# Kernel optimization log

Hardware: AMD Instinct MI355X
Metric: run time of the kernel (lower is better)

The kernel has to match this reference:

```python
import jax, jax.numpy as jnp
import numpy as np

D_IN = 1024
D_OUT = 1024
N_HEADS = 16
HEAD_DIM = D_IN // N_HEADS      # 64
HEAD_DIM_V = D_OUT // N_HEADS   # 64


def setup_inputs() -> dict:
    key = jax.random.key(0)
    ks = jax.random.split(key, 7)
    s = 0.02
    x = jax.random.normal(ks[0], (4, 2048, D_IN), dtype=jnp.float32)
    Wq = jax.random.normal(ks[1], (D_IN, D_IN), dtype=jnp.float32) * s
    bq = jnp.zeros((D_IN,), dtype=jnp.float32)
    Wk = jax.random.normal(ks[2], (D_IN, D_IN), dtype=jnp.float32) * s
    bk = jnp.zeros((D_IN,), dtype=jnp.float32)
    Wv = jax.random.normal(ks[3], (D_IN, D_OUT), dtype=jnp.float32) * s
    bv = jnp.zeros((D_OUT,), dtype=jnp.float32)
    return {"x": x, "Wq": Wq, "bq": bq, "Wk": Wk, "bk": bk, "Wv": Wv, "bv": bv}


def reference(x, Wq, bq, Wk, bk, Wv, bv):
    B, S, _ = x.shape
    scale = jnp.sqrt(jnp.asarray(HEAD_DIM, dtype=jnp.float32))
    # projections -> [B, S, H, Dh] -> [B, H, S, Dh]
    q = (x @ Wq + bq).reshape(B, S, N_HEADS, HEAD_DIM).transpose(0, 2, 1, 3)
    k = (x @ Wk + bk).reshape(B, S, N_HEADS, HEAD_DIM).transpose(0, 2, 1, 3)
    v = (x @ Wv + bv).reshape(B, S, N_HEADS, HEAD_DIM_V).transpose(0, 2, 1, 3)
    # [B, H, S, S] attention scores (naive full materialization, as in source)
    scores = jnp.einsum("bhsd,bhtd->bhst", q, k) / scale
    weights = jax.nn.softmax(scores, axis=-1)
    out = jnp.einsum("bhst,bhtd->bhsd", weights, v)
    # [B, H, S, Dv] -> [B, S, H*Dv]  (out_projection NOT applied in source forward)
    return out.transpose(0, 2, 1, 3).reshape(B, S, N_HEADS * HEAD_DIM_V)
```

## Files before the change

kernel.cpp:

```cpp
#include <hip/hip_runtime.h>

#define B_  4
#define S_  2048
#define D_  1024
#define H_  16
#define DH_ 64
#define M_  (B_ * S_)

typedef __attribute__((ext_vector_type(8))) short short8;
typedef __attribute__((ext_vector_type(4))) float floatx4;

__device__ __forceinline__ float bf2f(unsigned short u) {
    union { unsigned int i; float f; } v; v.i = ((unsigned int)u) << 16; return v.f;
}
__device__ __forceinline__ unsigned short f2bf(float f) {
    union { float f; unsigned int i; } v; v.f = f;
    unsigned int r = v.i + 0x7fffu + ((v.i >> 16) & 1u);
    return (unsigned short)(r >> 16);
}

typedef const __attribute__((address_space(1))) unsigned int* gas_ptr;
typedef __attribute__((address_space(3))) unsigned int* las_ptr;
__device__ __forceinline__ void async_cp16(const void* g, void* l) {
    __builtin_amdgcn_global_load_lds((gas_ptr)g, (las_ptr)l, 16, 0, 0);
}

__global__ __launch_bounds__(256) void cast_x_kernel(
    const float* __restrict__ x, unsigned short* __restrict__ Ax)
{
    int i4 = blockIdx.x * 256 + threadIdx.x;
    float4 v = reinterpret_cast<const float4*>(x)[i4];
    ushort4 o;
    o.x = f2bf(v.x); o.y = f2bf(v.y); o.z = f2bf(v.z); o.w = f2bf(v.w);
    reinterpret_cast<ushort4*>(Ax)[i4] = o;
}

__global__ __launch_bounds__(256) void cast_w_T_kernel(
    const float* __restrict__ W, unsigned short* __restrict__ Wt)
{
    __shared__ unsigned short T[64][72];
    const int t = threadIdx.x;
    const int k0 = blockIdx.x * 64, n0 = blockIdx.y * 64;

    #pragma unroll
    for (int p = 0; p < 4; ++p) {
        int kr = p * 16 + (t >> 4);
        int nc = (t & 15) * 4;
        float4 v = *reinterpret_cast<const float4*>(W + (size_t)(k0 + kr) * D_ + n0 + nc);
        T[nc + 0][kr] = f2bf(v.x);
        T[nc + 1][kr] = f2bf(v.y);
        T[nc + 2][kr] = f2bf(v.z);
        T[nc + 3][kr] = f2bf(v.w);
    }
    __syncthreads();

    const int nl = t >> 2, kc = (t & 3) * 16;
    size_t base = (size_t)(n0 + nl) * D_ + k0 + kc;
    *reinterpret_cast<short8*>(Wt + base)     = *reinterpret_cast<const short8*>(&T[nl][kc]);
    *reinterpret_cast<short8*>(Wt + base + 8) = *reinterpret_cast<const short8*>(&T[nl][kc + 8]);
}

__global__ __launch_bounds__(256) void gemm_qkv_mfma(
    const unsigned short* __restrict__ Ax,
    const unsigned short* __restrict__ Wtq,
    const unsigned short* __restrict__ Wtk,
    const unsigned short* __restrict__ Wtv,
    const float* __restrict__ bq, const float* __restrict__ bk,
    const float* __restrict__ bv,
    unsigned short* __restrict__ Q, unsigned short* __restrict__ K,
    unsigned short* __restrict__ Vtg)
{
    __shared__ unsigned short As[128 * 32];
    __shared__ unsigned short Bs[128 * 32];

    const int tid = threadIdx.x;
    const int lane = tid & 63;
    const int w = tid >> 6;
    const int wm = (w >> 1) * 64, wn = (w & 1) * 64;
    const int l15 = lane & 15, quad = lane >> 4;

    const int hw   = blockIdx.x;
    const int xcd  = hw & 7;
    const int slot = hw >> 3;
    const int gcol = xcd * 3 + slot % 3;
    const int m0   = (slot / 3) * 128;
    const int n0   = (gcol & 7) * 128;
    const int mat  = gcol >> 3;

    const unsigned short* Wt = mat == 0 ? Wtq : (mat == 1 ? Wtk : Wtv);
    const float* bias        = mat == 0 ? bq  : (mat == 1 ? bk  : bv);

    const int arow = tid >> 2;
    const int acol = (tid & 3) * 8;

    floatx4 acc[4][4] = {};

    for (int kb = 0; kb < 32; ++kb) {
        int cb = kb * 32;
        __syncthreads();
        async_cp16(Ax + (size_t)(m0 + arow) * D_ + cb + acol,      As + arow * 32 + acol);
        async_cp16(Ax + (size_t)(m0 + 64 + arow) * D_ + cb + acol, As + (64 + arow) * 32 + acol);
        async_cp16(Wt + (size_t)(n0 + arow) * D_ + cb + acol,      Bs + arow * 32 + acol);
        async_cp16(Wt + (size_t)(n0 + 64 + arow) * D_ + cb + acol, Bs + (64 + arow) * 32 + acol);
        __syncthreads();

        short8 af[4], bf[4];
        #pragma unroll
        for (int i = 0; i < 4; ++i)
            af[i] = *reinterpret_cast<const short8*>(As + (wm + i * 16 + l15) * 32 + quad * 8);
        #pragma unroll
        for (int j = 0; j < 4; ++j)
            bf[j] = *reinterpret_cast<const short8*>(Bs + (wn + j * 16 + l15) * 32 + quad * 8);
        #pragma unroll
        for (int i = 0; i < 4; ++i)
            #pragma unroll
            for (int j = 0; j < 4; ++j)
                acc[i][j] = __builtin_amdgcn_mfma_f32_16x16x32_bf16(af[i], bf[j], acc[i][j], 0, 0, 0);
    }

    float bb[4];
    #pragma unroll
    for (int j = 0; j < 4; ++j) bb[j] = bias[n0 + wn + j * 16 + l15];

    if (mat == 2) {
        const int b = m0 >> 11;
        #pragma unroll
        for (int i = 0; i < 4; ++i) {
            int srow = (m0 & 2047) + wm + i * 16 + quad * 4;
            #pragma unroll
            for (int j = 0; j < 4; ++j) {
                int col = n0 + wn + j * 16 + l15;
                ushort4 o;
                o.x = f2bf(acc[i][j][0] + bb[j]);
                o.y = f2bf(acc[i][j][1] + bb[j]);
                o.z = f2bf(acc[i][j][2] + bb[j]);
                o.w = f2bf(acc[i][j][3] + bb[j]);
                *reinterpret_cast<ushort4*>(Vtg + (size_t)(b * 1024 + col) * S_ + srow) = o;
            }
        }
    } else {
        unsigned short* C = (mat == 0) ? Q : K;
        const float sc = (mat == 0) ? 0.125f : 1.0f;
        #pragma unroll
        for (int i = 0; i < 4; ++i)
            #pragma unroll
            for (int r = 0; r < 4; ++r) {
                int row = m0 + wm + i * 16 + quad * 4 + r;
                #pragma unroll
                for (int j = 0; j < 4; ++j)
                    C[(size_t)row * D_ + n0 + wn + j * 16 + l15] = f2bf((acc[i][j][r] + bb[j]) * sc);
            }
    }
}

#define KT_   64
#define PITCH 72

__global__ __launch_bounds__(256) void attn_mfma(
    const unsigned short* __restrict__ Qg,
    const unsigned short* __restrict__ Kg,
    const unsigned short* __restrict__ Vtg,
    float* __restrict__ out)
{
    __shared__ unsigned short Ks[KT_ * PITCH];
    __shared__ unsigned short Vt[DH_ * PITCH];
    __shared__ unsigned short Ps[4][16 * PITCH];

    const int tid  = threadIdx.x;
    const int wq   = tid >> 6;
    const int lane = tid & 63;
    const int l15  = lane & 15;
    const int quad = lane >> 4;

    const int id  = blockIdx.x;
    const int bh  = (id & 7) * 8 + ((id >> 3) & 7);
    const int qt  = id >> 6;
    const int b   = bh >> 4;
    const int colbase = (bh & 15) * DH_;
    const int rowQ0 = b * S_ + qt * 128;

    short8 qf[2][2];
    #pragma unroll
    for (int g = 0; g < 2; ++g) {
        int qrow = rowQ0 + wq * 32 + g * 16 + l15;
        qf[g][0] = *reinterpret_cast<const short8*>(Qg + (size_t)qrow * D_ + colbase + quad * 8);
        qf[g][1] = *reinterpret_cast<const short8*>(Qg + (size_t)qrow * D_ + colbase + 32 + quad * 8);
    }

    floatx4 Oacc[2][4] = {};
    float lsum[2] = {0.f, 0.f};

    const int srow = tid >> 3;
    const int sc8  = (tid & 7) * 8;

    const unsigned short* Kbase = Kg + (size_t)(b * S_) * D_ + colbase;
    const unsigned short* Vbase = Vtg + (size_t)(bh * 64) * S_;

    short8 kpre[2], vpre[2];
    #pragma unroll
    for (int p = 0; p < 2; ++p) {
        kpre[p] = *reinterpret_cast<const short8*>(Kbase + (size_t)(p * 32 + srow) * D_ + sc8);
        vpre[p] = *reinterpret_cast<const short8*>(Vbase + (size_t)(p * 32 + srow) * S_ + sc8);
    }

    for (int kt = 0; kt < S_ / KT_; ++kt) {
        __syncthreads();
        #pragma unroll
        for (int p = 0; p < 2; ++p) {
            *reinterpret_cast<short8*>(&Ks[(p * 32 + srow) * PITCH + sc8]) = kpre[p];
            *reinterpret_cast<short8*>(&Vt[(p * 32 + srow) * PITCH + sc8]) = vpre[p];
        }
        if (kt + 1 < S_ / KT_) {
            int off = (kt + 1) * KT_;
            #pragma unroll
            for (int p = 0; p < 2; ++p) {
                kpre[p] = *reinterpret_cast<const short8*>(Kbase + (size_t)(off + p * 32 + srow) * D_ + sc8);
                vpre[p] = *reinterpret_cast<const short8*>(Vbase + (size_t)(p * 32 + srow) * S_ + off + sc8);
            }
        }
        __syncthreads();

        floatx4 sacc[2][4];
        #pragma unroll
        for (int c = 0; c < 4; ++c) {
            short8 kf0 = *reinterpret_cast<const short8*>(&Ks[(c * 16 + l15) * PITCH + quad * 8]);
            short8 kf1 = *reinterpret_cast<const short8*>(&Ks[(c * 16 + l15) * PITCH + 32 + quad * 8]);
            #pragma unroll
            for (int g = 0; g < 2; ++g) {
                floatx4 a = {0.f, 0.f, 0.f, 0.f};
                a = __builtin_amdgcn_mfma_f32_16x16x32_bf16(kf0, qf[g][0], a, 0, 0, 0);
                a = __builtin_amdgcn_mfma_f32_16x16x32_bf16(kf1, qf[g][1], a, 0, 0, 0);
                sacc[g][c] = a;
            }
        }

        short8 pf[2][2];
        #pragma unroll
        for (int g = 0; g < 2; ++g) {
            #pragma unroll
            for (int c = 0; c < 4; ++c) {
                float p0 = __expf(sacc[g][c][0]);
                float p1 = __expf(sacc[g][c][1]);
                float p2 = __expf(sacc[g][c][2]);
                float p3 = __expf(sacc[g][c][3]);
                lsum[g] += p0 + p1 + p2 + p3;
                ushort4 pk;
                pk.x = f2bf(p0); pk.y = f2bf(p1); pk.z = f2bf(p2); pk.w = f2bf(p3);
                *reinterpret_cast<ushort4*>(&Ps[wq][l15 * PITCH + c * 16 + quad * 4]) = pk;
            }
            pf[g][0] = *reinterpret_cast<const short8*>(&Ps[wq][l15 * PITCH + quad * 8]);
            pf[g][1] = *reinterpret_cast<const short8*>(&Ps[wq][l15 * PITCH + 32 + quad * 8]);
        }

        #pragma unroll
        for (int c = 0; c < 4; ++c) {
            short8 vf0 = *reinterpret_cast<const short8*>(&Vt[(c * 16 + l15) * PITCH + quad * 8]);
            short8 vf1 = *reinterpret_cast<const short8*>(&Vt[(c * 16 + l15) * PITCH + 32 + quad * 8]);
            #pragma unroll
            for (int g = 0; g < 2; ++g) {
                Oacc[g][c] = __builtin_amdgcn_mfma_f32_16x16x32_bf16(pf[g][0], vf0, Oacc[g][c], 0, 0, 0);
                Oacc[g][c] = __builtin_amdgcn_mfma_f32_16x16x32_bf16(pf[g][1], vf1, Oacc[g][c], 0, 0, 0);
            }
        }
    }

    #pragma unroll
    for (int g = 0; g < 2; ++g) {
        float lred = lsum[g];
        lred += __shfl_xor(lred, 16);
        lred += __shfl_xor(lred, 32);
        float inv[4];
        #pragma unroll
        for (int r = 0; r < 4; ++r)
            inv[r] = 1.f / __shfl(lred, quad * 4 + r);
        int orow = rowQ0 + wq * 32 + g * 16 + quad * 4;
        #pragma unroll
        for (int r = 0; r < 4; ++r)
            #pragma unroll
            for (int c = 0; c < 4; ++c)
                out[(size_t)(orow + r) * D_ + colbase + c * 16 + l15] = Oacc[g][c][r] * inv[r];
    }
}

extern "C" void kernel_launch(void* const* d_in, const int* in_sizes, int n_in,
                              void* d_out, int out_size, void* d_ws, size_t ws_size,
                              hipStream_t stream) {
    const float* x  = (const float*)d_in[0];
    const float* Wq = (const float*)d_in[1];
    const float* bq = (const float*)d_in[2];
    const float* Wk = (const float*)d_in[3];
    const float* bk = (const float*)d_in[4];
    const float* Wv = (const float*)d_in[5];
    const float* bv = (const float*)d_in[6];
    float* out = (float*)d_out;

    unsigned short* Q   = (unsigned short*)d_ws;
    unsigned short* K   = Q + (size_t)M_ * D_;
    unsigned short* Vtg = K + (size_t)M_ * D_;
    unsigned short* Ax  = Vtg + (size_t)M_ * D_;
    unsigned short* Wtq = Ax + (size_t)M_ * D_;
    unsigned short* Wtk = Wtq + (size_t)D_ * D_;
    unsigned short* Wtv = Wtk + (size_t)D_ * D_;

    cast_x_kernel<<<M_ * D_ / 4 / 256, 256, 0, stream>>>(x, Ax);
    dim3 gw(16, 16);
    cast_w_T_kernel<<<gw, 256, 0, stream>>>(Wq, Wtq);
    cast_w_T_kernel<<<gw, 256, 0, stream>>>(Wk, Wtk);
    cast_w_T_kernel<<<gw, 256, 0, stream>>>(Wv, Wtv);

    gemm_qkv_mfma<<<1536, 256, 0, stream>>>(Ax, Wtq, Wtk, Wtv, bq, bk, bv, Q, K, Vtg);

    attn_mfma<<<1024, 256, 0, stream>>>(Q, K, Vtg, out);
}
```

Before: 278.3 us.

## Keep P in registers via 16x16x16 MFMA, double query rows per block, remap GEMM tiles

```diff
diff --git a/kernel.cpp b/kernel.cpp
--- a/kernel.cpp
+++ b/kernel.cpp
@@ -8,6 +8,7 @@
 #define M_  (B_ * S_)
 
 typedef __attribute__((ext_vector_type(8))) short short8;
+typedef __attribute__((ext_vector_type(4))) short short4v;
 typedef __attribute__((ext_vector_type(4))) float floatx4;
 
 __device__ __forceinline__ float bf2f(unsigned short u) {
@@ -17,6 +18,9 @@
     union { float f; unsigned int i; } v; v.f = f;
     unsigned int r = v.i + 0x7fffu + ((v.i >> 16) & 1u);
     return (unsigned short)(r >> 16);
+}
+__device__ __forceinline__ unsigned int pk_trunc(float a, float b) {
+    return (__float_as_uint(a) >> 16) | (__float_as_uint(b) & 0xffff0000u);
 }
 
 typedef const __attribute__((address_space(1))) unsigned int* gas_ptr;
@@ -82,8 +86,9 @@
     const int hw   = blockIdx.x;
     const int xcd  = hw & 7;
     const int slot = hw >> 3;
-    const int gcol = xcd * 3 + slot % 3;
-    const int m0   = (slot / 3) * 128;
+    const int gcol = slot >> 3;
+    const int mi   = slot & 7;
+    const int m0   = (xcd * 8 + mi) * 128;
     const int n0   = (gcol & 7) * 128;
     const int mat  = gcol >> 3;
 
@@ -156,6 +161,12 @@
 #define KT_   64
 #define PITCH 72
 
+#if __has_builtin(__builtin_amdgcn_mfma_f32_16x16x16bf16_1k)
+#define PV_K16 1
+#else
+#define PV_K16 0
+#endif
+
 __global__ __launch_bounds__(256) void attn_mfma(
     const unsigned short* __restrict__ Qg,
     const unsigned short* __restrict__ Kg,
@@ -164,7 +175,9 @@
 {
     __shared__ unsigned short Ks[KT_ * PITCH];
     __shared__ unsigned short Vt[DH_ * PITCH];
+#if !PV_K16
     __shared__ unsigned short Ps[4][16 * PITCH];
+#endif
 
     const int tid  = threadIdx.x;
     const int wq   = tid >> 6;
@@ -177,18 +190,18 @@
     const int qt  = id >> 6;
     const int b   = bh >> 4;
     const int colbase = (bh & 15) * DH_;
-    const int rowQ0 = b * S_ + qt * 128;
-
-    short8 qf[2][2];
-    #pragma unroll
-    for (int g = 0; g < 2; ++g) {
-        int qrow = rowQ0 + wq * 32 + g * 16 + l15;
+    const int rowQ0 = b * S_ + qt * 256;
+
+    short8 qf[4][2];
+    #pragma unroll
+    for (int g = 0; g < 4; ++g) {
+        int qrow = rowQ0 + wq * 64 + g * 16 + l15;
         qf[g][0] = *reinterpret_cast<const short8*>(Qg + (size_t)qrow * D_ + colbase + quad * 8);
         qf[g][1] = *reinterpret_cast<const short8*>(Qg + (size_t)qrow * D_ + colbase + 32 + quad * 8);
     }
 
-    floatx4 Oacc[2][4] = {};
-    float lsum[2] = {0.f, 0.f};
+    floatx4 Oacc[4][4] = {};
+    float lsum[4] = {};
 
     const int srow = tid >> 3;
     const int sc8  = (tid & 7) * 8;
@@ -220,52 +233,79 @@
         }
         __syncthreads();
 
-        floatx4 sacc[2][4];
         #pragma unroll
         for (int c = 0; c < 4; ++c) {
             short8 kf0 = *reinterpret_cast<const short8*>(&Ks[(c * 16 + l15) * PITCH + quad * 8]);
             short8 kf1 = *reinterpret_cast<const short8*>(&Ks[(c * 16 + l15) * PITCH + 32 + quad * 8]);
-            #pragma unroll
-            for (int g = 0; g < 2; ++g) {
+            floatx4 sc_[4];
+            #pragma unroll
+            for (int g = 0; g < 4; ++g) {
                 floatx4 a = {0.f, 0.f, 0.f, 0.f};
                 a = __builtin_amdgcn_mfma_f32_16x16x32_bf16(kf0, qf[g][0], a, 0, 0, 0);
                 a = __builtin_amdgcn_mfma_f32_16x16x32_bf16(kf1, qf[g][1], a, 0, 0, 0);
-                sacc[g][c] = a;
-            }
-        }
-
-        short8 pf[2][2];
-        #pragma unroll
-        for (int g = 0; g < 2; ++g) {
-            #pragma unroll
-            for (int c = 0; c < 4; ++c) {
-                float p0 = __expf(sacc[g][c][0]);
-                float p1 = __expf(sacc[g][c][1]);
-                float p2 = __expf(sacc[g][c][2]);
-                float p3 = __expf(sacc[g][c][3]);
+                sc_[g] = a;
+            }
+
+#if PV_K16
+            short4v pfv[4];
+            #pragma unroll
+            for (int g = 0; g < 4; ++g) {
+                float p0 = __expf(sc_[g][0]);
+                float p1 = __expf(sc_[g][1]);
+                float p2 = __expf(sc_[g][2]);
+                float p3 = __expf(sc_[g][3]);
                 lsum[g] += p0 + p1 + p2 + p3;
-                ushort4 pk;
-                pk.x = f2bf(p0); pk.y = f2bf(p1); pk.z = f2bf(p2); pk.w = f2bf(p3);
-                *reinterpret_cast<ushort4*>(&Ps[wq][l15 * PITCH + c * 16 + quad * 4]) = pk;
-            }
-            pf[g][0] = *reinterpret_cast<const short8*>(&Ps[wq][l15 * PITCH + quad * 8]);
-            pf[g][1] = *reinterpret_cast<const short8*>(&Ps[wq][l15 * PITCH + 32 + quad * 8]);
-        }
-
-        #pragma unroll
-        for (int c = 0; c < 4; ++c) {
-            short8 vf0 = *reinterpret_cast<const short8*>(&Vt[(c * 16 + l15) * PITCH + quad * 8]);
-            short8 vf1 = *reinterpret_cast<const short8*>(&Vt[(c * 16 + l15) * PITCH + 32 + quad * 8]);
-            #pragma unroll
-            for (int g = 0; g < 2; ++g) {
-                Oacc[g][c] = __builtin_amdgcn_mfma_f32_16x16x32_bf16(pf[g][0], vf0, Oacc[g][c], 0, 0, 0);
-                Oacc[g][c] = __builtin_amdgcn_mfma_f32_16x16x32_bf16(pf[g][1], vf1, Oacc[g][c], 0, 0, 0);
-            }
-        }
-    }
-
-    #pragma unroll
-    for (int g = 0; g < 2; ++g) {
+                uint2 u;
+                u.x = pk_trunc(p0, p1);
+                u.y = pk_trunc(p2, p3);
+                pfv[g] = __builtin_bit_cast(short4v, u);
+            }
+            #pragma unroll
+            for (int d = 0; d < 4; ++d) {
+                short4v vf = *reinterpret_cast<const short4v*>(
+                    &Vt[(d * 16 + l15) * PITCH + c * 16 + quad * 4]);
+                #pragma unroll
+                for (int g = 0; g < 4; ++g)
+                    Oacc[g][d] = __builtin_amdgcn_mfma_f32_16x16x16bf16_1k(
+                        pfv[g], vf, Oacc[g][d], 0, 0, 0);
+            }
+#else
+            #pragma unroll
+            for (int g = 0; g < 4; ++g) {
+                float p0 = __expf(sc_[g][0]);
+                float p1 = __expf(sc_[g][1]);
+                float p2 = __expf(sc_[g][2]);
+                float p3 = __expf(sc_[g][3]);
+                lsum[g] += p0 + p1 + p2 + p3;
+                uint2 u;
+                u.x = pk_trunc(p0, p1);
+                u.y = pk_trunc(p2, p3);
+                *reinterpret_cast<uint2*>(&Ps[wq][(l15 + g * 0) * PITCH + c * 16 + quad * 4]) = u;
+                short8 pf0 = *reinterpret_cast<const short8*>(&Ps[wq][l15 * PITCH + quad * 8]);
+                short8 pf1 = *reinterpret_cast<const short8*>(&Ps[wq][l15 * PITCH + 32 + quad * 8]);
+                (void)pf0; (void)pf1;
+            }
+#endif
+        }
+
+#if !PV_K16
+        #pragma unroll
+        for (int g = 0; g < 4; ++g) {
+            short8 pf0 = *reinterpret_cast<const short8*>(&Ps[wq][l15 * PITCH + quad * 8]);
+            short8 pf1 = *reinterpret_cast<const short8*>(&Ps[wq][l15 * PITCH + 32 + quad * 8]);
+            #pragma unroll
+            for (int d = 0; d < 4; ++d) {
+                short8 vf0 = *reinterpret_cast<const short8*>(&Vt[(d * 16 + l15) * PITCH + quad * 8]);
+                short8 vf1 = *reinterpret_cast<const short8*>(&Vt[(d * 16 + l15) * PITCH + 32 + quad * 8]);
+                Oacc[g][d] = __builtin_amdgcn_mfma_f32_16x16x32_bf16(pf0, vf0, Oacc[g][d], 0, 0, 0);
+                Oacc[g][d] = __builtin_amdgcn_mfma_f32_16x16x32_bf16(pf1, vf1, Oacc[g][d], 0, 0, 0);
+            }
+        }
+#endif
+    }
+
+    #pragma unroll
+    for (int g = 0; g < 4; ++g) {
         float lred = lsum[g];
         lred += __shfl_xor(lred, 16);
         lred += __shfl_xor(lred, 32);
@@ -273,12 +313,12 @@
         #pragma unroll
         for (int r = 0; r < 4; ++r)
             inv[r] = 1.f / __shfl(lred, quad * 4 + r);
-        int orow = rowQ0 + wq * 32 + g * 16 + quad * 4;
+        int orow = rowQ0 + wq * 64 + g * 16 + quad * 4;
         #pragma unroll
         for (int r = 0; r < 4; ++r)
             #pragma unroll
-            for (int c = 0; c < 4; ++c)
-                out[(size_t)(orow + r) * D_ + colbase + c * 16 + l15] = Oacc[g][c][r] * inv[r];
+            for (int d = 0; d < 4; ++d)
+                out[(size_t)(orow + r) * D_ + colbase + d * 16 + l15] = Oacc[g][d][r] * inv[r];
     }
 }
 
@@ -310,5 +350,5 @@
 
     gemm_qkv_mfma<<<1536, 256, 0, stream>>>(Ax, Wtq, Wtk, Wtv, bq, bk, bv, Q, K, Vtg);
 
-    attn_mfma<<<1024, 256, 0, stream>>>(Q, K, Vtg, out);
-}
+    attn_mfma<<<512, 256, 0, stream>>>(Q, K, Vtg, out);
+}
```

After: 279.4 us. Within noise of the previous version (+0.4%).

## Keep softmax probabilities in registers via permuted V layout, drop P LDS round-trip

Applied to the files above, without the earlier changes.

```diff
diff --git a/kernel.cpp b/kernel.cpp
--- a/kernel.cpp
+++ b/kernel.cpp
@@ -17,6 +17,9 @@
     union { float f; unsigned int i; } v; v.f = f;
     unsigned int r = v.i + 0x7fffu + ((v.i >> 16) & 1u);
     return (unsigned short)(r >> 16);
+}
+__device__ __forceinline__ unsigned int pk_trunc(float a, float b) {
+    return (__float_as_uint(a) >> 16) | (__float_as_uint(b) & 0xffff0000u);
 }
 
 typedef const __attribute__((address_space(1))) unsigned int* gas_ptr;
@@ -82,8 +85,9 @@
     const int hw   = blockIdx.x;
     const int xcd  = hw & 7;
     const int slot = hw >> 3;
-    const int gcol = xcd * 3 + slot % 3;
-    const int m0   = (slot / 3) * 128;
+    const int gcol = slot >> 3;
+    const int mi   = slot & 7;
+    const int m0   = (xcd * 8 + mi) * 128;
     const int n0   = (gcol & 7) * 128;
     const int mat  = gcol >> 3;
 
@@ -156,7 +160,7 @@
 #define KT_   64
 #define PITCH 72
 
-__global__ __launch_bounds__(256) void attn_mfma(
+__global__ __launch_bounds__(256, 4) void attn_mfma(
     const unsigned short* __restrict__ Qg,
     const unsigned short* __restrict__ Kg,
     const unsigned short* __restrict__ Vtg,
@@ -164,7 +168,6 @@
 {
     __shared__ unsigned short Ks[KT_ * PITCH];
     __shared__ unsigned short Vt[DH_ * PITCH];
-    __shared__ unsigned short Ps[4][16 * PITCH];
 
     const int tid  = threadIdx.x;
     const int wq   = tid >> 6;
@@ -192,6 +195,9 @@
 
     const int srow = tid >> 3;
     const int sc8  = (tid & 7) * 8;
+    const int vc  = sc8 >> 4;
+    const int vqk = (sc8 >> 2) & 3;
+    const int vk0 = ((vc & 1) << 2) + ((vc >> 1) << 5) + (vqk << 3);
 
     const unsigned short* Kbase = Kg + (size_t)(b * S_) * D_ + colbase;
     const unsigned short* Vbase = Vtg + (size_t)(bh * 64) * S_;
@@ -208,7 +214,11 @@
         #pragma unroll
         for (int p = 0; p < 2; ++p) {
             *reinterpret_cast<short8*>(&Ks[(p * 32 + srow) * PITCH + sc8]) = kpre[p];
-            *reinterpret_cast<short8*>(&Vt[(p * 32 + srow) * PITCH + sc8]) = vpre[p];
+            uint4 u = __builtin_bit_cast(uint4, vpre[p]);
+            uint2 lo, hi;
+            lo.x = u.x; lo.y = u.y; hi.x = u.z; hi.y = u.w;
+            *reinterpret_cast<uint2*>(&Vt[(p * 32 + srow) * PITCH + vk0])     = lo;
+            *reinterpret_cast<uint2*>(&Vt[(p * 32 + srow) * PITCH + vk0 + 8]) = hi;
         }
         if (kt + 1 < S_ / KT_) {
             int off = (kt + 1) * KT_;
@@ -220,46 +230,44 @@
         }
         __syncthreads();
 
-        floatx4 sacc[2][4];
-        #pragma unroll
-        for (int c = 0; c < 4; ++c) {
-            short8 kf0 = *reinterpret_cast<const short8*>(&Ks[(c * 16 + l15) * PITCH + quad * 8]);
-            short8 kf1 = *reinterpret_cast<const short8*>(&Ks[(c * 16 + l15) * PITCH + 32 + quad * 8]);
+        #pragma unroll
+        for (int half = 0; half < 2; ++half) {
+            floatx4 s_[2][2];
+            #pragma unroll
+            for (int ci = 0; ci < 2; ++ci) {
+                int c = half * 2 + ci;
+                short8 kf0 = *reinterpret_cast<const short8*>(&Ks[(c * 16 + l15) * PITCH + quad * 8]);
+                short8 kf1 = *reinterpret_cast<const short8*>(&Ks[(c * 16 + l15) * PITCH + 32 + quad * 8]);
+                #pragma unroll
+                for (int g = 0; g < 2; ++g) {
+                    floatx4 a = {0.f, 0.f, 0.f, 0.f};
+                    a = __builtin_amdgcn_mfma_f32_16x16x32_bf16(kf0, qf[g][0], a, 0, 0, 0);
+                    a = __builtin_amdgcn_mfma_f32_16x16x32_bf16(kf1, qf[g][1], a, 0, 0, 0);
+                    s_[g][ci] = a;
+                }
+            }
+            short8 pa[2];
             #pragma unroll
             for (int g = 0; g < 2; ++g) {
-                floatx4 a = {0.f, 0.f, 0.f, 0.f};
-                a = __builtin_amdgcn_mfma_f32_16x16x32_bf16(kf0, qf[g][0], a, 0, 0, 0);
-                a = __builtin_amdgcn_mfma_f32_16x16x32_bf16(kf1, qf[g][1], a, 0, 0, 0);
-                sacc[g][c] = a;
-            }
-        }
-
-        short8 pf[2][2];
-        #pragma unroll
-        for (int g = 0; g < 2; ++g) {
-            #pragma unroll
-            for (int c = 0; c < 4; ++c) {
-                float p0 = __expf(sacc[g][c][0]);
-                float p1 = __expf(sacc[g][c][1]);
-                float p2 = __expf(sacc[g][c][2]);
-                float p3 = __expf(sacc[g][c][3]);
-                lsum[g] += p0 + p1 + p2 + p3;
-                ushort4 pk;
-                pk.x = f2bf(p0); pk.y = f2bf(p1); pk.z = f2bf(p2); pk.w = f2bf(p3);
-                *reinterpret_cast<ushort4*>(&Ps[wq][l15 * PITCH + c * 16 + quad * 4]) = pk;
-            }
-            pf[g][0] = *reinterpret_cast<const short8*>(&Ps[wq][l15 * PITCH + quad * 8]);
-            pf[g][1] = *reinterpret_cast<const short8*>(&Ps[wq][l15 * PITCH + 32 + quad * 8]);
-        }
-
-        #pragma unroll
-        for (int c = 0; c < 4; ++c) {
-            short8 vf0 = *reinterpret_cast<const short8*>(&Vt[(c * 16 + l15) * PITCH + quad * 8]);
-            short8 vf1 = *reinterpret_cast<const short8*>(&Vt[(c * 16 + l15) * PITCH + 32 + quad * 8]);
-            #pragma unroll
-            for (int g = 0; g < 2; ++g) {
-                Oacc[g][c] = __builtin_amdgcn_mfma_f32_16x16x32_bf16(pf[g][0], vf0, Oacc[g][c], 0, 0, 0);
-                Oacc[g][c] = __builtin_amdgcn_mfma_f32_16x16x32_bf16(pf[g][1], vf1, Oacc[g][c], 0, 0, 0);
+                float p00 = __expf(s_[g][0][0]), p01 = __expf(s_[g][0][1]);
+                float p02 = __expf(s_[g][0][2]), p03 = __expf(s_[g][0][3]);
+                float p10 = __expf(s_[g][1][0]), p11 = __expf(s_[g][1][1]);
+                float p12 = __expf(s_[g][1][2]), p13 = __expf(s_[g][1][3]);
+                lsum[g] += (p00 + p01) + (p02 + p03) + (p10 + p11) + (p12 + p13);
+                uint4 pu;
+                pu.x = pk_trunc(p00, p01);
+                pu.y = pk_trunc(p02, p03);
+                pu.z = pk_trunc(p10, p11);
+                pu.w = pk_trunc(p12, p13);
+                pa[g] = __builtin_bit_cast(short8, pu);
+            }
+            #pragma unroll
+            for (int d = 0; d < 4; ++d) {
+                short8 vf = *reinterpret_cast<const short8*>(
+                    &Vt[(d * 16 + l15) * PITCH + half * 32 + quad * 8]);
+                #pragma unroll
+                for (int g = 0; g < 2; ++g)
+                    Oacc[g][d] = __builtin_amdgcn_mfma_f32_16x16x32_bf16(pa[g], vf, Oacc[g][d], 0, 0, 0);
             }
         }
     }
@@ -277,8 +285,8 @@
         #pragma unroll
         for (int r = 0; r < 4; ++r)
             #pragma unroll
-            for (int c = 0; c < 4; ++c)
-                out[(size_t)(orow + r) * D_ + colbase + c * 16 + l15] = Oacc[g][c][r] * inv[r];
+            for (int d = 0; d < 4; ++d)
+                out[(size_t)(orow + r) * D_ + colbase + d * 16 + l15] = Oacc[g][d][r] * inv[r];
     }
 }
 
```

Measured after the change: 251.7 us. -9.5%, faster.
